# Optimization experiments

Hardware: AMD Instinct MI355X
Metric: run time of the kernel (lower is better)

The kernel has to match this reference:

```python
import jax, jax.numpy as jnp
import numpy as np

EMBED = 1024
HEADS = 16
HEAD_DIM = EMBED // HEADS


def setup_inputs() -> dict:
    key = jax.random.key(0)
    ks = jax.random.split(key, 6)
    N, S = 4, 1024
    query = jax.random.normal(ks[0], (N, S, EMBED), dtype=jnp.float32)
    keys = jax.random.normal(ks[1], (N, S, EMBED), dtype=jnp.float32)
    values = jax.random.normal(ks[2], (N, S, EMBED), dtype=jnp.float32)
    mask = jax.random.randint(ks[3], (N, 1, S, S), 0, 2, dtype=jnp.int32)
    W_out = jax.random.normal(ks[4], (EMBED, EMBED), dtype=jnp.float32) * (1.0 / np.sqrt(EMBED))
    b_out = jax.random.normal(ks[5], (EMBED,), dtype=jnp.float32) * 0.02
    return {"query": query, "keys": keys, "values": values, "mask": mask,
            "W_out": W_out, "b_out": b_out}


def reference(query, keys, values, mask, W_out, b_out):
    N, Q, _ = query.shape
    K = keys.shape[1]
    # NOTE: the torch module never applies its per-head q/k/v Linear layers;
    # only the reshape + attention + fc_out are in the forward path.
    q = query.reshape(N, Q, HEADS, HEAD_DIM)
    k = keys.reshape(N, K, HEADS, HEAD_DIM)
    v = values.reshape(N, K, HEADS, HEAD_DIM)
    # energy: [N, H, Q, K]
    energy = jnp.einsum("bqhd,bkhd->bhqk", q, k)
    energy = jnp.where(mask == 0, jnp.float32(-1e20), energy)
    attn = jax.nn.softmax(energy / jnp.sqrt(jnp.float32(HEAD_DIM)), axis=3)
    out = jnp.einsum("bhqk,bkhd->bqhd", attn, v).reshape(N, Q, HEADS * HEAD_DIM)
    return out @ W_out.T + b_out
```

## Files before the change

### kernel.cpp

```cpp
#include <hip/hip_runtime.h>
#include <math.h>

#define NB 4
#define SL 1024
#define EMB 1024
#define NH 16
#define HD 64
#define QB 128

typedef __attribute__((ext_vector_type(8))) short bf16x8;
typedef __attribute__((ext_vector_type(4))) float f32x4;

static __device__ __forceinline__ unsigned pk2(float a, float b) {
    unsigned x = __float_as_uint(a) + 0x8000u;
    unsigned y = __float_as_uint(b) + 0x8000u;
    return (x >> 16) | (y & 0xFFFF0000u);
}
static __device__ __forceinline__ float exp2_fast(float x) {
    float r; asm("v_exp_f32 %0, %1" : "=v"(r) : "v"(x)); return r;
}
static __device__ __forceinline__ void gload_lds16(const void* g, void* l) {
    __builtin_amdgcn_global_load_lds(
        (const __attribute__((address_space(1))) unsigned int*)g,
        (__attribute__((address_space(3))) unsigned int*)l, 16, 0, 0);
}

__global__ void mprep(const int* __restrict__ mask, unsigned long long* __restrict__ Mbt) {
    int wid  = blockIdx.x * 4 + (threadIdx.x >> 6);
    int lane = threadIdx.x & 63;
    int c = wid & 15, q = (wid >> 4) & 1023, bb = wid >> 14;
    int mv = mask[((size_t)bb * SL + q) * SL + c * 64 + lane];
    unsigned long long bits = __ballot(mv != 0);
    if (lane == 0) Mbt[((size_t)bb * 16 + c) * SL + q] = bits;
}

__global__ void wprep(const float* __restrict__ W, unsigned short* __restrict__ Wb) {
    int i = (blockIdx.x * 256 + threadIdx.x) * 8;
    float4 f0 = *(const float4*)&W[i];
    float4 f1 = *(const float4*)&W[i + 4];
    uint4 u = { pk2(f0.x,f0.y), pk2(f0.z,f0.w), pk2(f1.x,f1.y), pk2(f1.z,f1.w) };
    *(uint4*)&Wb[i] = u;
}

__global__ void vprep(const float* __restrict__ V, unsigned short* __restrict__ Vt) {
    __shared__ unsigned short sT[128 * 68];
    const int bh = blockIdx.x, kb = blockIdx.y, tid = threadIdx.x;
    const int b = bh >> 4, h = bh & 15;
    const int k0 = kb * 128;
    #pragma unroll
    for (int i = 0; i < 4; ++i) {
        int lin = (i * 256 + tid) * 8;
        int r = lin >> 6, d = lin & 63;
        const float* gp = &V[((size_t)(b * SL + k0 + r)) * EMB + h * HD + d];
        float4 f0 = *(const float4*)gp, f1 = *(const float4*)(gp + 4);
        uint2 u0 = { pk2(f0.x,f0.y), pk2(f0.z,f0.w) };
        uint2 u1 = { pk2(f1.x,f1.y), pk2(f1.z,f1.w) };
        *(uint2*)&sT[r * 68 + d]     = u0;
        *(uint2*)&sT[r * 68 + d + 4] = u1;
    }
    __syncthreads();
    #pragma unroll
    for (int p = 0; p < 4; ++p) {
        int d = p * 16 + (tid >> 4);
        int c = tid & 15;
        unsigned v[4];
        #pragma unroll
        for (int j = 0; j < 4; ++j) {
            unsigned lo = sT[(c * 8 + 2 * j) * 68 + d];
            unsigned hi = sT[(c * 8 + 2 * j + 1) * 68 + d];
            v[j] = lo | (hi << 16);
        }
        uint4 u = { v[0], v[1], v[2], v[3] };
        *(uint4*)&Vt[((size_t)(bh * HD + d)) * SL + k0 + c * 8] = u;
    }
}

__global__ __launch_bounds__(256, 2) void attn_mfma(
    const float* __restrict__ Q, const float* __restrict__ K,
    const unsigned short* __restrict__ Vt,
    const unsigned long long* __restrict__ Mbt,
    unsigned short* __restrict__ Oa)
{
    const int q0 = blockIdx.x * QB;
    const int h = blockIdx.y, b = blockIdx.z;
    const int tid = threadIdx.x;
    const int w = tid >> 6, lane = tid & 63;
    const int m16 = lane & 15, quad = lane >> 4;
    const int lr = lane >> 3, lc = lane & 7;

    __shared__ __align__(16) unsigned short sQ[QB * 64];
    __shared__ __align__(16) unsigned short sK[2][64 * 64];
    __shared__ __align__(16) unsigned short sVt[2][64 * 64];
    __shared__ __align__(16) unsigned short sP[QB * 72];
    __shared__ uint2 lut[16];

    if (tid < 16) {
        unsigned w0 = ((tid & 1) ? 0xFFFFu : 0u) | ((tid & 2) ? 0xFFFF0000u : 0u);
        unsigned w1 = ((tid & 4) ? 0xFFFFu : 0u) | ((tid & 8) ? 0xFFFF0000u : 0u);
        lut[tid] = make_uint2(w0, w1);
    }

    const size_t vbase = (size_t)((b * NH + h) * HD) * SL;
    const int sr0 = tid >> 3;

    #pragma unroll
    for (int i = 0; i < 2; ++i) {
        int row = w * 16 + i * 8;
        gload_lds16(&Vt[vbase + (size_t)(row + lr) * SL + (lc ^ lr) * 8], &sVt[0][row * 64]);
    }
    float4 kr[4];
    #pragma unroll
    for (int it = 0; it < 2; ++it) {
        int r = sr0 + it * 32;
        const float* gp = &K[((size_t)(b * SL + r)) * EMB + h * HD + lc * 8];
        kr[2*it]   = *(const float4*)gp;
        kr[2*it+1] = *(const float4*)(gp + 4);
    }
    #pragma unroll
    for (int it = 0; it < 4; ++it) {
        int r = sr0 + it * 32;
        const float* gp = &Q[((size_t)(b * SL + q0 + r)) * EMB + h * HD + lc * 8];
        float4 f0 = *(const float4*)gp, f1 = *(const float4*)(gp + 4);
        uint4 u = { pk2(f0.x,f0.y), pk2(f0.z,f0.w), pk2(f1.x,f1.y), pk2(f1.z,f1.w) };
        *(uint4*)&sQ[r * 64 + ((lc ^ (r & 7)) * 8)] = u;
    }
    #pragma unroll
    for (int it = 0; it < 2; ++it) {
        int r = sr0 + it * 32;
        uint4 u = { pk2(kr[2*it].x, kr[2*it].y),     pk2(kr[2*it].z, kr[2*it].w),
                    pk2(kr[2*it+1].x, kr[2*it+1].y), pk2(kr[2*it+1].z, kr[2*it+1].w) };
        *(uint4*)&sK[0][r * 64 + ((lc ^ (r & 7)) * 8)] = u;
    }
    __syncthreads();

    bf16x8 bQ[2][2];
    #pragma unroll
    for (int u = 0; u < 2; ++u) {
        int qrow = w * 32 + u * 16 + m16;
        #pragma unroll
        for (int hh = 0; hh < 2; ++hh)
            bQ[u][hh] = *(const bf16x8*)&sQ[qrow * 64 + (((hh * 4 + quad) ^ (qrow & 7)) * 8)];
    }

    f32x4 O[2][4] = {};
    f32x4 lacc[2] = {};
    const float CSC = 0.125f * 1.44269504f;
    const short one_bf = (short)0x3F80;
    const bf16x8 ones = { one_bf, one_bf, one_bf, one_bf, one_bf, one_bf, one_bf, one_bf };

    for (int kt = 0; kt < 16; ++kt) {
        const int bf = kt & 1;
        if (kt < 15) {
            const int k0n = (kt + 1) * 64;
            #pragma unroll
            for (int i = 0; i < 2; ++i) {
                int row = w * 16 + i * 8;
                gload_lds16(&Vt[vbase + (size_t)(row + lr) * SL + k0n + (lc ^ lr) * 8],
                            &sVt[bf ^ 1][row * 64]);
            }
            #pragma unroll
            for (int it = 0; it < 2; ++it) {
                int r = sr0 + it * 32;
                const float* gp = &K[((size_t)(b * SL + k0n + r)) * EMB + h * HD + lc * 8];
                kr[2*it]   = *(const float4*)gp;
                kr[2*it+1] = *(const float4*)(gp + 4);
            }
        }
        unsigned long long mb0 = Mbt[(size_t)(b * 16 + kt) * SL + q0 + w * 32 + m16];
        unsigned long long mb1 = Mbt[(size_t)(b * 16 + kt) * SL + q0 + w * 32 + 16 + m16];

        f32x4 sc[2][4];
        #pragma unroll
        for (int t = 0; t < 4; ++t) {
            int krow = t * 16 + m16;
            bf16x8 a0 = *(const bf16x8*)&sK[bf][krow * 64 + ((quad ^ (krow & 7)) * 8)];
            bf16x8 a1 = *(const bf16x8*)&sK[bf][krow * 64 + (((4 + quad) ^ (krow & 7)) * 8)];
            f32x4 z = {0.f, 0.f, 0.f, 0.f};
            sc[0][t] = __builtin_amdgcn_mfma_f32_16x16x32_bf16(a0, bQ[0][0], z,        0,0,0);
            sc[0][t] = __builtin_amdgcn_mfma_f32_16x16x32_bf16(a1, bQ[0][1], sc[0][t], 0,0,0);
            sc[1][t] = __builtin_amdgcn_mfma_f32_16x16x32_bf16(a0, bQ[1][0], z,        0,0,0);
            sc[1][t] = __builtin_amdgcn_mfma_f32_16x16x32_bf16(a1, bQ[1][1], sc[1][t], 0,0,0);
        }

        #pragma unroll
        for (int u = 0; u < 2; ++u) {
            unsigned long long mb = u ? mb1 : mb0;
            unsigned wlo = (unsigned)mb, whi = (unsigned)(mb >> 32);
            unsigned short* pr = &sP[(w * 32 + u * 16 + m16) * 72];
            #pragma unroll
            for (int t = 0; t < 4; ++t) {
                unsigned word = (t < 2) ? wlo : whi;
                unsigned nib = (word >> ((t & 1) * 16 + quad * 4)) & 0xFu;
                uint2 am = lut[nib];
                uint2 pw;
                pw.x = pk2(exp2_fast(sc[u][t][0] * CSC), exp2_fast(sc[u][t][1] * CSC)) & am.x;
                pw.y = pk2(exp2_fast(sc[u][t][2] * CSC), exp2_fast(sc[u][t][3] * CSC)) & am.y;
                *(uint2*)&pr[t * 16 + quad * 4] = pw;
            }
        }
        asm volatile("s_waitcnt lgkmcnt(0)" ::: "memory");

        bf16x8 bP[2][2];
        #pragma unroll
        for (int u = 0; u < 2; ++u)
            #pragma unroll
            for (int hh = 0; hh < 2; ++hh)
                bP[u][hh] = *(const bf16x8*)&sP[(w * 32 + u * 16 + m16) * 72 + hh * 32 + quad * 8];

        lacc[0] = __builtin_amdgcn_mfma_f32_16x16x32_bf16(ones, bP[0][0], lacc[0], 0,0,0);
        lacc[0] = __builtin_amdgcn_mfma_f32_16x16x32_bf16(ones, bP[0][1], lacc[0], 0,0,0);
        lacc[1] = __builtin_amdgcn_mfma_f32_16x16x32_bf16(ones, bP[1][0], lacc[1], 0,0,0);
        lacc[1] = __builtin_amdgcn_mfma_f32_16x16x32_bf16(ones, bP[1][1], lacc[1], 0,0,0);

        #pragma unroll
        for (int dt = 0; dt < 4; ++dt) {
            int drow = dt * 16 + m16;
            bf16x8 v0 = *(const bf16x8*)&sVt[bf][drow * 64 + ((quad ^ (drow & 7)) * 8)];
            bf16x8 v1 = *(const bf16x8*)&sVt[bf][drow * 64 + (((4 + quad) ^ (drow & 7)) * 8)];
            O[0][dt] = __builtin_amdgcn_mfma_f32_16x16x32_bf16(v0, bP[0][0], O[0][dt], 0,0,0);
            O[0][dt] = __builtin_amdgcn_mfma_f32_16x16x32_bf16(v1, bP[0][1], O[0][dt], 0,0,0);
            O[1][dt] = __builtin_amdgcn_mfma_f32_16x16x32_bf16(v0, bP[1][0], O[1][dt], 0,0,0);
            O[1][dt] = __builtin_amdgcn_mfma_f32_16x16x32_bf16(v1, bP[1][1], O[1][dt], 0,0,0);
        }

        if (kt < 15) {
            #pragma unroll
            for (int it = 0; it < 2; ++it) {
                int r = sr0 + it * 32;
                uint4 u = { pk2(kr[2*it].x, kr[2*it].y),     pk2(kr[2*it].z, kr[2*it].w),
                            pk2(kr[2*it+1].x, kr[2*it+1].y), pk2(kr[2*it+1].z, kr[2*it+1].w) };
                *(uint4*)&sK[bf ^ 1][r * 64 + ((lc ^ (r & 7)) * 8)] = u;
            }
        }
        __syncthreads();
    }

    #pragma unroll
    for (int u = 0; u < 2; ++u) {
        float inv = 1.f / lacc[u][0];
        size_t base = ((size_t)(b * SL + q0 + w * 32 + u * 16 + m16)) * EMB + h * HD + quad * 4;
        #pragma unroll
        for (int dt = 0; dt < 4; ++dt) {
            uint2 ow = { pk2(O[u][dt][0] * inv, O[u][dt][1] * inv),
                         pk2(O[u][dt][2] * inv, O[u][dt][3] * inv) };
            *(uint2*)&Oa[base + dt * 16] = ow;
        }
    }
}

__global__ __launch_bounds__(512, 2) void proj_mfma(
    const unsigned short* __restrict__ A, const unsigned short* __restrict__ Wb,
    const float* __restrict__ bias, float* __restrict__ C)
{
    const int n0 = blockIdx.x * 128;
    const int m0 = blockIdx.y * 128;
    const int tid = threadIdx.x;
    const int w = tid >> 6, lane = tid & 63;
    const int m16 = lane & 15, quad = lane >> 4;
    const int lr = lane >> 3, lc = lane & 7;
    const int wm = (w >> 2) * 64, wn = (w & 3) * 32;

    __shared__ __align__(16) unsigned short sA[2][128 * 64];
    __shared__ __align__(16) unsigned short sW[2][128 * 64];

    f32x4 acc[4][2] = {};

    #pragma unroll
    for (int i = 0; i < 2; ++i) {
        int r = w * 16 + i * 8;
        gload_lds16(&A [(size_t)(m0 + r + lr) * EMB + (lc ^ lr) * 8], &sA[0][r * 64]);
        gload_lds16(&Wb[(size_t)(n0 + r + lr) * EMB + (lc ^ lr) * 8], &sW[0][r * 64]);
    }
    __syncthreads();

    for (int it = 0; it < 16; ++it) {
        const int bf = it & 1;
        if (it < 15) {
            int e0 = (it + 1) * 64;
            #pragma unroll
            for (int i = 0; i < 2; ++i) {
                int r = w * 16 + i * 8;
                gload_lds16(&A [(size_t)(m0 + r + lr) * EMB + e0 + (lc ^ lr) * 8], &sA[bf ^ 1][r * 64]);
                gload_lds16(&Wb[(size_t)(n0 + r + lr) * EMB + e0 + (lc ^ lr) * 8], &sW[bf ^ 1][r * 64]);
            }
        }
        #pragma unroll
        for (int hh = 0; hh < 2; ++hh) {
            bf16x8 af[4], bw[2];
            #pragma unroll
            for (int mt = 0; mt < 4; ++mt) {
                int r = wm + mt * 16 + m16;
                af[mt] = *(const bf16x8*)&sA[bf][r * 64 + (((hh * 4 + quad) ^ (r & 7)) * 8)];
            }
            #pragma unroll
            for (int nt = 0; nt < 2; ++nt) {
                int r = wn + nt * 16 + m16;
                bw[nt] = *(const bf16x8*)&sW[bf][r * 64 + (((hh * 4 + quad) ^ (r & 7)) * 8)];
            }
            #pragma unroll
            for (int mt = 0; mt < 4; ++mt)
                #pragma unroll
                for (int nt = 0; nt < 2; ++nt)
                    acc[mt][nt] = __builtin_amdgcn_mfma_f32_16x16x32_bf16(af[mt], bw[nt], acc[mt][nt], 0,0,0);
        }
        __syncthreads();
    }

    #pragma unroll
    for (int nt = 0; nt < 2; ++nt) {
        float bv = bias[n0 + wn + nt * 16 + m16];
        #pragma unroll
        for (int mt = 0; mt < 4; ++mt) {
            size_t row = (size_t)(m0 + wm + mt * 16 + quad * 4);
            #pragma unroll
            for (int rg = 0; rg < 4; ++rg)
                C[(row + rg) * EMB + n0 + wn + nt * 16 + m16] = acc[mt][nt][rg] + bv;
        }
    }
}

extern "C" void kernel_launch(void* const* d_in, const int* in_sizes, int n_in,
                              void* d_out, int out_size, void* d_ws, size_t ws_size,
                              hipStream_t stream) {
    const float* Q    = (const float*)d_in[0];
    const float* K    = (const float*)d_in[1];
    const float* V    = (const float*)d_in[2];
    const int*   mask = (const int*)  d_in[3];
    const float* W    = (const float*)d_in[4];
    const float* bias = (const float*)d_in[5];

    unsigned short* Oa = (unsigned short*)d_ws;
    unsigned short* Wb = Oa + (size_t)NB * SL * EMB;
    unsigned long long* Mbt = (unsigned long long*)(Wb + (size_t)EMB * EMB);
    unsigned short* Vt = (unsigned short*)(Mbt + (size_t)NB * 16 * SL);

    wprep<<<EMB * EMB / (256 * 8), 256, 0, stream>>>(W, Wb);
    mprep<<<NB * SL * 16 / 4, 256, 0, stream>>>(mask, Mbt);
    vprep<<<dim3(NB * NH, SL / 128), 256, 0, stream>>>(V, Vt);
    attn_mfma<<<dim3(SL / QB, NH, NB), 256, 0, stream>>>(Q, K, Vt, Mbt, Oa);
    proj_mfma<<<dim3(EMB / 128, (NB * SL) / 128), 512, 0, stream>>>(Oa, Wb, bias, (float*)d_out);
}
```

Measured before the change: 174.9 us.

## Merge prep kernels into one launch and pre-convert K to bf16 head-major layout

```diff
diff --git a/kernel.cpp b/kernel.cpp
--- a/kernel.cpp
+++ b/kernel.cpp
@@ -25,58 +25,76 @@
         (__attribute__((address_space(3))) unsigned int*)l, 16, 0, 0);
 }
 
-__global__ void mprep(const int* __restrict__ mask, unsigned long long* __restrict__ Mbt) {
-    int wid  = blockIdx.x * 4 + (threadIdx.x >> 6);
-    int lane = threadIdx.x & 63;
-    int c = wid & 15, q = (wid >> 4) & 1023, bb = wid >> 14;
-    int mv = mask[((size_t)bb * SL + q) * SL + c * 64 + lane];
-    unsigned long long bits = __ballot(mv != 0);
-    if (lane == 0) Mbt[((size_t)bb * 16 + c) * SL + q] = bits;
-}
-
-__global__ void wprep(const float* __restrict__ W, unsigned short* __restrict__ Wb) {
-    int i = (blockIdx.x * 256 + threadIdx.x) * 8;
-    float4 f0 = *(const float4*)&W[i];
-    float4 f1 = *(const float4*)&W[i + 4];
-    uint4 u = { pk2(f0.x,f0.y), pk2(f0.z,f0.w), pk2(f1.x,f1.y), pk2(f1.z,f1.w) };
-    *(uint4*)&Wb[i] = u;
-}
-
-__global__ void vprep(const float* __restrict__ V, unsigned short* __restrict__ Vt) {
+__global__ __launch_bounds__(256) void prep(
+    const float* __restrict__ W, unsigned short* __restrict__ Wb,
+    const float* __restrict__ Kf, unsigned short* __restrict__ Kb,
+    const float* __restrict__ V, unsigned short* __restrict__ Vt,
+    const int* __restrict__ mask, unsigned long long* __restrict__ Mbt)
+{
     __shared__ unsigned short sT[128 * 68];
-    const int bh = blockIdx.x, kb = blockIdx.y, tid = threadIdx.x;
-    const int b = bh >> 4, h = bh & 15;
-    const int k0 = kb * 128;
-    #pragma unroll
-    for (int i = 0; i < 4; ++i) {
-        int lin = (i * 256 + tid) * 8;
-        int r = lin >> 6, d = lin & 63;
-        const float* gp = &V[((size_t)(b * SL + k0 + r)) * EMB + h * HD + d];
+    const int bid = blockIdx.x, tid = threadIdx.x;
+
+    if (bid < 512) {
+        int i = (bid * 256 + tid) * 8;
+        float4 f0 = *(const float4*)&W[i];
+        float4 f1 = *(const float4*)&W[i + 4];
+        uint4 u = { pk2(f0.x,f0.y), pk2(f0.z,f0.w), pk2(f1.x,f1.y), pk2(f1.z,f1.w) };
+        *(uint4*)&Wb[i] = u;
+    } else if (bid < 2560) {
+        int t = bid - 512;
+        int b = t >> 9, h = (t >> 5) & 15, k0 = (t & 31) * 32;
+        int r = tid >> 3, d = (tid & 7) * 8;
+        const float* gp = &Kf[((size_t)(b * SL + k0 + r)) * EMB + h * HD + d];
         float4 f0 = *(const float4*)gp, f1 = *(const float4*)(gp + 4);
-        uint2 u0 = { pk2(f0.x,f0.y), pk2(f0.z,f0.w) };
-        uint2 u1 = { pk2(f1.x,f1.y), pk2(f1.z,f1.w) };
-        *(uint2*)&sT[r * 68 + d]     = u0;
-        *(uint2*)&sT[r * 68 + d + 4] = u1;
-    }
-    __syncthreads();
-    #pragma unroll
-    for (int p = 0; p < 4; ++p) {
-        int d = p * 16 + (tid >> 4);
-        int c = tid & 15;
-        unsigned v[4];
-        #pragma unroll
-        for (int j = 0; j < 4; ++j) {
-            unsigned lo = sT[(c * 8 + 2 * j) * 68 + d];
-            unsigned hi = sT[(c * 8 + 2 * j + 1) * 68 + d];
-            v[j] = lo | (hi << 16);
-        }
-        uint4 u = { v[0], v[1], v[2], v[3] };
-        *(uint4*)&Vt[((size_t)(bh * HD + d)) * SL + k0 + c * 8] = u;
+        uint4 u = { pk2(f0.x,f0.y), pk2(f0.z,f0.w), pk2(f1.x,f1.y), pk2(f1.z,f1.w) };
+        *(uint4*)&Kb[((size_t)((b * NH + h) * SL + k0 + r)) * HD + d] = u;
+    } else if (bid < 3072) {
+        int t = bid - 2560;
+        int bh = t >> 3, kb = t & 7;
+        int b = bh >> 4, h = bh & 15;
+        int k0 = kb * 128;
+        #pragma unroll
+        for (int i = 0; i < 4; ++i) {
+            int lin = (i * 256 + tid) * 8;
+            int r = lin >> 6, d = lin & 63;
+            const float* gp = &V[((size_t)(b * SL + k0 + r)) * EMB + h * HD + d];
+            float4 f0 = *(const float4*)gp, f1 = *(const float4*)(gp + 4);
+            uint2 u0 = { pk2(f0.x,f0.y), pk2(f0.z,f0.w) };
+            uint2 u1 = { pk2(f1.x,f1.y), pk2(f1.z,f1.w) };
+            *(uint2*)&sT[r * 68 + d]     = u0;
+            *(uint2*)&sT[r * 68 + d + 4] = u1;
+        }
+        __syncthreads();
+        #pragma unroll
+        for (int p = 0; p < 4; ++p) {
+            int d = p * 16 + (tid >> 4);
+            int c = tid & 15;
+            unsigned v[4];
+            #pragma unroll
+            for (int j = 0; j < 4; ++j) {
+                unsigned lo = sT[(c * 8 + 2 * j) * 68 + d];
+                unsigned hi = sT[(c * 8 + 2 * j + 1) * 68 + d];
+                v[j] = lo | (hi << 16);
+            }
+            uint4 u = { v[0], v[1], v[2], v[3] };
+            *(uint4*)&Vt[((size_t)(bh * HD + d)) * SL + k0 + c * 8] = u;
+        }
+    } else {
+        int t = bid - 3072;
+        int lane = tid & 63;
+        #pragma unroll
+        for (int r = 0; r < 4; ++r) {
+            int wid = (t * 4 + (tid >> 6)) * 4 + r;
+            int c = wid & 15, q = (wid >> 4) & 1023, bb = wid >> 14;
+            int mv = mask[((size_t)bb * SL + q) * SL + c * 64 + lane];
+            unsigned long long bits = __ballot(mv != 0);
+            if (lane == 0) Mbt[((size_t)bb * 16 + c) * SL + q] = bits;
+        }
     }
 }
 
 __global__ __launch_bounds__(256, 2) void attn_mfma(
-    const float* __restrict__ Q, const float* __restrict__ K,
+    const float* __restrict__ Q, const unsigned short* __restrict__ Kb,
     const unsigned short* __restrict__ Vt,
     const unsigned long long* __restrict__ Mbt,
     unsigned short* __restrict__ Oa)
@@ -87,6 +105,7 @@
     const int w = tid >> 6, lane = tid & 63;
     const int m16 = lane & 15, quad = lane >> 4;
     const int lr = lane >> 3, lc = lane & 7;
+    const int sr0 = tid >> 3;
 
     __shared__ __align__(16) unsigned short sQ[QB * 64];
     __shared__ __align__(16) unsigned short sK[2][64 * 64];
@@ -101,20 +120,13 @@
     }
 
     const size_t vbase = (size_t)((b * NH + h) * HD) * SL;
-    const int sr0 = tid >> 3;
+    const size_t kbase = (size_t)((b * NH + h) * SL) * HD;
 
     #pragma unroll
     for (int i = 0; i < 2; ++i) {
         int row = w * 16 + i * 8;
         gload_lds16(&Vt[vbase + (size_t)(row + lr) * SL + (lc ^ lr) * 8], &sVt[0][row * 64]);
-    }
-    float4 kr[4];
-    #pragma unroll
-    for (int it = 0; it < 2; ++it) {
-        int r = sr0 + it * 32;
-        const float* gp = &K[((size_t)(b * SL + r)) * EMB + h * HD + lc * 8];
-        kr[2*it]   = *(const float4*)gp;
-        kr[2*it+1] = *(const float4*)(gp + 4);
+        gload_lds16(&Kb[kbase + (size_t)(row + lr) * HD + (lc ^ lr) * 8], &sK[0][row * 64]);
     }
     #pragma unroll
     for (int it = 0; it < 4; ++it) {
@@ -124,13 +136,6 @@
         uint4 u = { pk2(f0.x,f0.y), pk2(f0.z,f0.w), pk2(f1.x,f1.y), pk2(f1.z,f1.w) };
         *(uint4*)&sQ[r * 64 + ((lc ^ (r & 7)) * 8)] = u;
     }
-    #pragma unroll
-    for (int it = 0; it < 2; ++it) {
-        int r = sr0 + it * 32;
-        uint4 u = { pk2(kr[2*it].x, kr[2*it].y),     pk2(kr[2*it].z, kr[2*it].w),
-                    pk2(kr[2*it+1].x, kr[2*it+1].y), pk2(kr[2*it+1].z, kr[2*it+1].w) };
-        *(uint4*)&sK[0][r * 64 + ((lc ^ (r & 7)) * 8)] = u;
-    }
     __syncthreads();
 
     bf16x8 bQ[2][2];
@@ -157,13 +162,8 @@
                 int row = w * 16 + i * 8;
                 gload_lds16(&Vt[vbase + (size_t)(row + lr) * SL + k0n + (lc ^ lr) * 8],
                             &sVt[bf ^ 1][row * 64]);
-            }
-            #pragma unroll
-            for (int it = 0; it < 2; ++it) {
-                int r = sr0 + it * 32;
-                const float* gp = &K[((size_t)(b * SL + k0n + r)) * EMB + h * HD + lc * 8];
-                kr[2*it]   = *(const float4*)gp;
-                kr[2*it+1] = *(const float4*)(gp + 4);
+                gload_lds16(&Kb[kbase + (size_t)(k0n + row + lr) * HD + (lc ^ lr) * 8],
+                            &sK[bf ^ 1][row * 64]);
             }
         }
         unsigned long long mb0 = Mbt[(size_t)(b * 16 + kt) * SL + q0 + w * 32 + m16];
@@ -223,15 +223,6 @@
             O[1][dt] = __builtin_amdgcn_mfma_f32_16x16x32_bf16(v1, bP[1][1], O[1][dt], 0,0,0);
         }
 
-        if (kt < 15) {
-            #pragma unroll
-            for (int it = 0; it < 2; ++it) {
-                int r = sr0 + it * 32;
-                uint4 u = { pk2(kr[2*it].x, kr[2*it].y),     pk2(kr[2*it].z, kr[2*it].w),
-                            pk2(kr[2*it+1].x, kr[2*it+1].y), pk2(kr[2*it+1].z, kr[2*it+1].w) };
-                *(uint4*)&sK[bf ^ 1][r * 64 + ((lc ^ (r & 7)) * 8)] = u;
-            }
-        }
         __syncthreads();
     }
 
@@ -333,10 +324,9 @@
     unsigned short* Wb = Oa + (size_t)NB * SL * EMB;
     unsigned long long* Mbt = (unsigned long long*)(Wb + (size_t)EMB * EMB);
     unsigned short* Vt = (unsigned short*)(Mbt + (size_t)NB * 16 * SL);
-
-    wprep<<<EMB * EMB / (256 * 8), 256, 0, stream>>>(W, Wb);
-    mprep<<<NB * SL * 16 / 4, 256, 0, stream>>>(mask, Mbt);
-    vprep<<<dim3(NB * NH, SL / 128), 256, 0, stream>>>(V, Vt);
-    attn_mfma<<<dim3(SL / QB, NH, NB), 256, 0, stream>>>(Q, K, Vt, Mbt, Oa);
+    unsigned short* Kb = Vt + (size_t)NB * NH * HD * SL;
+
+    prep<<<7168, 256, 0, stream>>>(W, Wb, K, Kb, V, Vt, mask, Mbt);
+    attn_mfma<<<dim3(SL / QB, NH, NB), 256, 0, stream>>>(Q, Kb, Vt, Mbt, Oa);
     proj_mfma<<<dim3(EMB / 128, (NB * SL) / 128), 512, 0, stream>>>(Oa, Wb, bias, (float*)d_out);
 }
```

New measurement: 166.0 us. -5.1%, faster.
